# Optimization experiments

Measured on AMD Instinct MI355X. Metric: run time of the kernel, lower is better.

The kernel has to match this reference:

```python
import jax, jax.numpy as jnp
import numpy as np

N_BINS = 15
N, C = 1000000, 128


def setup_inputs() -> dict:
    key = jax.random.key(0)
    k1, k2 = jax.random.split(key)
    logits = jax.random.normal(k1, (N, C), dtype=jnp.float32)
    labels = jax.random.randint(k2, (N,), 0, C, dtype=jnp.int32)
    return {"logits": logits, "labels": labels}


def reference(logits, labels):
    # softmax + confidence/prediction (single pass, no [N,C] score re-materialization beyond probs)
    probs = jax.nn.softmax(logits, axis=1)            # [N, C]
    conf = jnp.max(probs, axis=1)                     # [N]
    pred = jnp.argmax(probs, axis=1)                  # [N]
    acc = (pred == labels).astype(conf.dtype)         # [N]

    # bin i covers (i/n_bins, (i+1)/n_bins]; searchsorted(uppers, conf, 'left')
    # gives the smallest j with uppers[j] >= conf, i.e. conf <= upper and conf > lower
    uppers = jnp.linspace(0.0, 1.0, N_BINS + 1, dtype=conf.dtype)[1:]  # [n_bins]
    bin_idx = jnp.clip(jnp.searchsorted(uppers, conf, side="left"), 0, N_BINS - 1)

    # fused histogram / segment reduce replacing the per-bin python loop
    counts = jax.ops.segment_sum(jnp.ones_like(conf), bin_idx, num_segments=N_BINS)
    sum_conf = jax.ops.segment_sum(conf, bin_idx, num_segments=N_BINS)
    sum_acc = jax.ops.segment_sum(acc, bin_idx, num_segments=N_BINS)

    nonempty = counts > 0
    safe = jnp.where(nonempty, counts, jnp.ones_like(counts))
    avg_conf = sum_conf / safe                        # per-bin avg confidence
    avg_acc = sum_acc / safe                          # per-bin accuracy

    gap = jnp.abs(avg_conf - avg_acc)
    # max over non-empty bins only (original skips bins with prop_in_bin == 0)
    mce = jnp.max(jnp.where(nonempty, gap, -jnp.inf))

    prob = jnp.where(nonempty, avg_conf, jnp.zeros_like(avg_conf))
    accu = jnp.where(nonempty, avg_acc, jnp.zeros_like(avg_acc))
    return mce, prob, accu
```

## Files before the change

### kernel.cpp

```cpp
#include <hip/hip_runtime.h>

#define NBINS 15

template <int CTRL>
__device__ __forceinline__ float dpp_mov_f(float v) {
    return __int_as_float(__builtin_amdgcn_update_dpp(
        __float_as_int(v), __float_as_int(v), CTRL, 0xF, 0xF, false));
}

__device__ __forceinline__ float half_reduce_max(float v) {
    v = fmaxf(v, dpp_mov_f<0xB1>(v));
    v = fmaxf(v, dpp_mov_f<0x4E>(v));
    v = fmaxf(v, dpp_mov_f<0x141>(v));
    v = fmaxf(v, dpp_mov_f<0x140>(v));
    v = fmaxf(v, dpp_mov_f<0x142>(v));
    return v;
}
__device__ __forceinline__ float half_reduce_sum(float v) {
    v += dpp_mov_f<0xB1>(v);
    v += dpp_mov_f<0x4E>(v);
    v += dpp_mov_f<0x141>(v);
    v += dpp_mov_f<0x140>(v);
    v += dpp_mov_f<0x142>(v);
    return v;
}

__global__ __launch_bounds__(256, 8) void mce_pass1(
    const float* __restrict__ logits, const int* __restrict__ labels,
    unsigned long long* __restrict__ conf_part,
    unsigned int* __restrict__ cnt_part,
    unsigned int* __restrict__ acc_part,
    int n)
{
    __shared__ unsigned int s_cnt[NBINS];
    __shared__ unsigned int s_acc[NBINS];
    __shared__ unsigned long long s_conf[NBINS];
    if (threadIdx.x < NBINS) {
        s_cnt[threadIdx.x] = 0u;
        s_acc[threadIdx.x] = 0u;
        s_conf[threadIdx.x] = 0ULL;
    }
    __syncthreads();

    const int lane32 = threadIdx.x & 31;
    const int half   = (threadIdx.x >> 5) & 1;
    const int hw_global = blockIdx.x * 8 + (threadIdx.x >> 5);
    const int hw_total  = gridDim.x * 8;
    const int B = gridDim.x;

    for (int row = hw_global; row < n; row += hw_total) {
        const float4 v = *(const float4*)(logits + (size_t)row * 128 + lane32 * 4);
        const int lab = labels[row];

        float m4 = fmaxf(fmaxf(v.x, v.y), fmaxf(v.z, v.w));
        float Mr = half_reduce_max(m4);
        const float MA = __int_as_float(__builtin_amdgcn_readlane(__float_as_int(Mr), 31));
        const float MB = __int_as_float(__builtin_amdgcn_readlane(__float_as_int(Mr), 63));
        const float Mh = half ? MB : MA;

        float e = __expf(v.x - Mh) + __expf(v.y - Mh) + __expf(v.z - Mh) + __expf(v.w - Mh);
        float Sr = half_reduce_sum(e);
        const int SA = __builtin_amdgcn_readlane(__float_as_int(Sr), 31);
        const int SB = __builtin_amdgcn_readlane(__float_as_int(Sr), 63);

        int idx_local = (v.x == Mh) ? 0 : (v.y == Mh) ? 1 : (v.z == Mh) ? 2 : 3;
        unsigned long long bal = __ballot(m4 == Mh);
        unsigned lo = (unsigned)bal;
        unsigned hi = (unsigned)(bal >> 32);
        int winA = __ffs(lo) - 1;
        int winB = __ffs(hi) - 1;
        int predA = (winA << 2) + __builtin_amdgcn_readlane(idx_local, winA);
        int predB = (winB << 2) + __builtin_amdgcn_readlane(idx_local, winB + 32);

        if (lane32 == 0) {
            float Sh = __int_as_float(half ? SB : SA);
            int pred = half ? predB : predA;
            float conf = 1.0f / Sh;
            int bin = (int)ceilf(conf * 15.0f) - 1;
            bin = max(0, min(NBINS - 1, bin));
            unsigned int acc = (pred == lab) ? 1u : 0u;
            unsigned int cb = __float_as_uint(conf);
            unsigned int mant = (cb & 0x7fffffu) | 0x800000u;
            int sh = (int)(cb >> 23) - 118;
            unsigned long long fc = (sh >= 0)
                ? ((unsigned long long)mant << sh)
                : ((unsigned long long)mant >> (-sh));
            atomicAdd(&s_cnt[bin], 1u);
            atomicAdd(&s_acc[bin], acc);
            atomicAdd(&s_conf[bin], fc);
        }
    }
    __syncthreads();
    if (threadIdx.x < NBINS) {
        cnt_part[threadIdx.x * B + blockIdx.x]  = s_cnt[threadIdx.x];
        acc_part[threadIdx.x * B + blockIdx.x]  = s_acc[threadIdx.x];
        conf_part[(size_t)threadIdx.x * B + blockIdx.x] = s_conf[threadIdx.x];
    }
}

__global__ __launch_bounds__(960) void mce_pass2(
    const unsigned long long* __restrict__ conf_part,
    const unsigned int* __restrict__ cnt_part,
    const unsigned int* __restrict__ acc_part,
    int B, float* __restrict__ out)
{
    __shared__ float s_prob[NBINS], s_accu[NBINS], s_gap[NBINS];
    __shared__ int s_ne[NBINS];

    const int bin  = threadIdx.x >> 6;
    const int lane = threadIdx.x & 63;

    unsigned long long csum = 0ULL;
    unsigned int cn = 0u, ac = 0u;
    #pragma unroll 4
    for (int i = lane; i < B; i += 64) {
        csum += conf_part[(size_t)bin * B + i];
        cn   += cnt_part[bin * B + i];
        ac   += acc_part[bin * B + i];
    }
    #pragma unroll
    for (int off = 32; off >= 1; off >>= 1) {
        csum += __shfl_xor(csum, off, 64);
        cn   += __shfl_xor(cn, off, 64);
        ac   += __shfl_xor(ac, off, 64);
    }

    if (lane == 0) {
        if (cn > 0u) {
            float p = (float)(((double)csum * (1.0 / 4294967296.0)) / (double)cn);
            float a = (float)((double)ac / (double)cn);
            s_prob[bin] = p;
            s_accu[bin] = a;
            s_gap[bin]  = fabsf(p - a);
            s_ne[bin]   = 1;
        } else {
            s_prob[bin] = 0.0f;
            s_accu[bin] = 0.0f;
            s_gap[bin]  = 0.0f;
            s_ne[bin]   = 0;
        }
    }
    __syncthreads();

    if (threadIdx.x == 0) {
        float mce = -1e30f;
        for (int b = 0; b < NBINS; ++b)
            if (s_ne[b] && s_gap[b] > mce) mce = s_gap[b];
        out[0] = mce;
    }
    if (threadIdx.x < NBINS) {
        out[1 + threadIdx.x]  = s_prob[threadIdx.x];
        out[16 + threadIdx.x] = s_accu[threadIdx.x];
    }
}

extern "C" void kernel_launch(void* const* d_in, const int* in_sizes, int n_in,
                              void* d_out, int out_size, void* d_ws, size_t ws_size,
                              hipStream_t stream) {
    const float* logits = (const float*)d_in[0];
    const int*   labels = (const int*)d_in[1];
    const int n = in_sizes[1];

    int B = 2048;
    const size_t per_block = (size_t)NBINS * (8 + 4 + 4);
    if ((size_t)B * per_block > ws_size) B = (int)(ws_size / per_block);
    if (B < 1) B = 1;

    unsigned long long* conf_part = (unsigned long long*)d_ws;
    unsigned int* cnt_part = (unsigned int*)((char*)d_ws + (size_t)B * NBINS * 8);
    unsigned int* acc_part = (unsigned int*)((char*)d_ws + (size_t)B * NBINS * 12);

    mce_pass1<<<B, 256, 0, stream>>>(logits, labels, conf_part, cnt_part, acc_part, n);
    mce_pass2<<<1, 960, 0, stream>>>(conf_part, cnt_part, acc_part, B, (float*)d_out);
}
```

Baseline: 664.5 us.

## Batch four rows per half-wave and keep bin histograms in per-lane registers

Each half-wave now loads four consecutive rows' logits plus a vectorized int4 of labels before processing any of them. This raises memory-level parallelism and amortizes loop overhead. Per-row shared-memory atomics are replaced by register accumulators, where lane i owns bin i. These are flushed to shared memory once per thread at the end. The cost is higher register pressure and a scalar tail loop for rows not divisible by four.

```diff
diff --git a/kernel.cpp b/kernel.cpp
--- a/kernel.cpp
+++ b/kernel.cpp
@@ -23,6 +23,49 @@
     v += dpp_mov_f<0x140>(v);
     v += dpp_mov_f<0x142>(v);
     return v;
+}
+
+__device__ __forceinline__ void process_row(
+    const float4 v, const int lab, const int lane32, const int half,
+    unsigned int& cnt_r, unsigned int& acc_r, unsigned long long& conf_r)
+{
+    float m4 = fmaxf(fmaxf(v.x, v.y), fmaxf(v.z, v.w));
+    float Mr = half_reduce_max(m4);
+    const float MA = __int_as_float(__builtin_amdgcn_readlane(__float_as_int(Mr), 31));
+    const float MB = __int_as_float(__builtin_amdgcn_readlane(__float_as_int(Mr), 63));
+    const float Mh = half ? MB : MA;
+
+    float e = __expf(v.x - Mh) + __expf(v.y - Mh) + __expf(v.z - Mh) + __expf(v.w - Mh);
+    float Sr = half_reduce_sum(e);
+    const int SAi = __builtin_amdgcn_readlane(__float_as_int(Sr), 31);
+    const int SBi = __builtin_amdgcn_readlane(__float_as_int(Sr), 63);
+    const float Sh = __int_as_float(half ? SBi : SAi);
+
+    int idx_local = (v.x == Mh) ? 0 : (v.y == Mh) ? 1 : (v.z == Mh) ? 2 : 3;
+    unsigned long long bal = __ballot(m4 == Mh);
+    unsigned lo = (unsigned)bal;
+    unsigned hi = (unsigned)(bal >> 32);
+    int winA = __ffs(lo) - 1;
+    int winB = __ffs(hi) - 1;
+    int predA = (winA << 2) + __builtin_amdgcn_readlane(idx_local, winA);
+    int predB = (winB << 2) + __builtin_amdgcn_readlane(idx_local, winB + 32);
+    const int pred = half ? predB : predA;
+
+    float conf = 1.0f / Sh;
+    int bin = (int)ceilf(conf * 15.0f) - 1;
+    bin = max(0, min(NBINS - 1, bin));
+    unsigned int acc = (pred == lab) ? 1u : 0u;
+    unsigned int cb = __float_as_uint(conf);
+    unsigned int mant = (cb & 0x7fffffu) | 0x800000u;
+    int sh = (int)(cb >> 23) - 118;
+    unsigned long long fc = (sh >= 0)
+        ? ((unsigned long long)mant << sh)
+        : ((unsigned long long)mant >> (-sh));
+
+    const bool own = (lane32 < NBINS) && (bin == lane32);
+    cnt_r  += own ? 1u : 0u;
+    acc_r  += own ? acc : 0u;
+    conf_r += own ? fc : 0ULL;
 }
 
 __global__ __launch_bounds__(256, 8) void mce_pass1(
@@ -48,47 +91,32 @@
     const int hw_total  = gridDim.x * 8;
     const int B = gridDim.x;
 
-    for (int row = hw_global; row < n; row += hw_total) {
-        const float4 v = *(const float4*)(logits + (size_t)row * 128 + lane32 * 4);
-        const int lab = labels[row];
-
-        float m4 = fmaxf(fmaxf(v.x, v.y), fmaxf(v.z, v.w));
-        float Mr = half_reduce_max(m4);
-        const float MA = __int_as_float(__builtin_amdgcn_readlane(__float_as_int(Mr), 31));
-        const float MB = __int_as_float(__builtin_amdgcn_readlane(__float_as_int(Mr), 63));
-        const float Mh = half ? MB : MA;
-
-        float e = __expf(v.x - Mh) + __expf(v.y - Mh) + __expf(v.z - Mh) + __expf(v.w - Mh);
-        float Sr = half_reduce_sum(e);
-        const int SA = __builtin_amdgcn_readlane(__float_as_int(Sr), 31);
-        const int SB = __builtin_amdgcn_readlane(__float_as_int(Sr), 63);
-
-        int idx_local = (v.x == Mh) ? 0 : (v.y == Mh) ? 1 : (v.z == Mh) ? 2 : 3;
-        unsigned long long bal = __ballot(m4 == Mh);
-        unsigned lo = (unsigned)bal;
-        unsigned hi = (unsigned)(bal >> 32);
-        int winA = __ffs(lo) - 1;
-        int winB = __ffs(hi) - 1;
-        int predA = (winA << 2) + __builtin_amdgcn_readlane(idx_local, winA);
-        int predB = (winB << 2) + __builtin_amdgcn_readlane(idx_local, winB + 32);
-
-        if (lane32 == 0) {
-            float Sh = __int_as_float(half ? SB : SA);
-            int pred = half ? predB : predA;
-            float conf = 1.0f / Sh;
-            int bin = (int)ceilf(conf * 15.0f) - 1;
-            bin = max(0, min(NBINS - 1, bin));
-            unsigned int acc = (pred == lab) ? 1u : 0u;
-            unsigned int cb = __float_as_uint(conf);
-            unsigned int mant = (cb & 0x7fffffu) | 0x800000u;
-            int sh = (int)(cb >> 23) - 118;
-            unsigned long long fc = (sh >= 0)
-                ? ((unsigned long long)mant << sh)
-                : ((unsigned long long)mant >> (-sh));
-            atomicAdd(&s_cnt[bin], 1u);
-            atomicAdd(&s_acc[bin], acc);
-            atomicAdd(&s_conf[bin], fc);
-        }
+    unsigned int cnt_r = 0u, acc_r = 0u;
+    unsigned long long conf_r = 0ULL;
+
+    const int stride = hw_total * 4;
+    int r0 = hw_global * 4;
+    for (; r0 + 4 <= n; r0 += stride) {
+        const float* base = logits + (size_t)r0 * 128 + lane32 * 4;
+        const float4 v0 = *(const float4*)(base);
+        const float4 v1 = *(const float4*)(base + 128);
+        const float4 v2 = *(const float4*)(base + 256);
+        const float4 v3 = *(const float4*)(base + 384);
+        const int4 lab4 = *(const int4*)(labels + r0);
+        process_row(v0, lab4.x, lane32, half, cnt_r, acc_r, conf_r);
+        process_row(v1, lab4.y, lane32, half, cnt_r, acc_r, conf_r);
+        process_row(v2, lab4.z, lane32, half, cnt_r, acc_r, conf_r);
+        process_row(v3, lab4.w, lane32, half, cnt_r, acc_r, conf_r);
+    }
+    for (; r0 < n; ++r0) {
+        const float4 v = *(const float4*)(logits + (size_t)r0 * 128 + lane32 * 4);
+        process_row(v, labels[r0], lane32, half, cnt_r, acc_r, conf_r);
+    }
+
+    if (lane32 < NBINS) {
+        atomicAdd(&s_cnt[lane32], cnt_r);
+        atomicAdd(&s_acc[lane32], acc_r);
+        atomicAdd(&s_conf[lane32], conf_r);
     }
     __syncthreads();
     if (threadIdx.x < NBINS) {
```

After: 672.7 us. About the same (+1.2%).
